# Performance work log

Hardware: AMD Instinct MI355X
Metric: run time of the kernel (lower is better)

The kernel has to match this reference:

```python
import jax, jax.numpy as jnp
import numpy as np

C = 512          # in_channels == key_channels
K_REGIONS = 256  # number of proxy/object regions
N, H, Wd = 8, 128, 128


def _cba(x, w, sc, bi):
    """1x1 Conv + (folded) BN + ReLU. x: [n, Cin, h, w], w: [Cout, Cin]."""
    y = jnp.einsum('nchw,oc->nohw', x, w)
    return jax.nn.relu(sc[None, :, None, None] * y + bi[None, :, None, None])


def setup_inputs() -> dict:
    key = jax.random.key(0)
    kx, kp, kw, ks, kb = jax.random.split(key, 5)
    x = jax.random.normal(kx, (N, C, H, Wd), dtype=jnp.float32)
    proxy = jax.random.normal(kp, (N, C, K_REGIONS, 1), dtype=jnp.float32)
    # 7 ConvBnAct layers: [fp0, fp1, fo0, fo1, fd0, fd1, fup]
    W = jax.random.normal(kw, (7, C, C), dtype=jnp.float32) * (1.0 / np.sqrt(C))
    s = jax.random.uniform(ks, (7, C), dtype=jnp.float32, minval=0.5, maxval=1.5)
    b = jax.random.normal(kb, (7, C), dtype=jnp.float32) * 0.02
    return {'x': x, 'proxy': proxy, 'W': W, 's': s, 'b': b}


def reference(x, proxy, W, s, b):
    n, _, h, w = x.shape
    # f_pixel(x): two 1x1 ConvBnAct -> query [n, HW, C]
    q = _cba(_cba(x, W[0], s[0], b[0]), W[1], s[1], b[1])
    query = q.reshape(n, C, h * w).transpose(0, 2, 1)          # [n, HW, C]
    # f_object(proxy) -> key [n, C, K]
    k = _cba(_cba(proxy, W[2], s[2], b[2]), W[3], s[3], b[3])
    key_t = k.reshape(n, C, -1)                                 # [n, C, K]
    # f_down(proxy) -> value [n, K, C]
    v = _cba(_cba(proxy, W[4], s[4], b[4]), W[5], s[5], b[5])
    value = v.reshape(n, C, -1).transpose(0, 2, 1)              # [n, K, C]
    # scaled dot-product attention (single head, unmasked)
    sim = jnp.einsum('nqc,nck->nqk', query, key_t) * (C ** -0.5)
    sim = jax.nn.softmax(sim, axis=-1)                          # [n, HW, K]
    context = jnp.einsum('nqk,nkc->nqc', sim, value)            # [n, HW, C]
    context = context.transpose(0, 2, 1).reshape(n, C, h, w)
    # f_up
    return _cba(context, W[6], s[6], b[6])
```

## Files before the change

### kernel.cpp

```cpp
#include <hip/hip_runtime.h>
#include <hip/hip_bf16.h>
#include <stdint.h>

typedef __bf16 bf16;
typedef __bf16 bf16x8 __attribute__((ext_vector_type(8)));
typedef __bf16 bf16x4v __attribute__((ext_vector_type(4)));
typedef float f32x4 __attribute__((ext_vector_type(4)));

#define AS1 __attribute__((address_space(1)))
#define AS3 __attribute__((address_space(3)))

__device__ __forceinline__ void g2lds16(const bf16* g, bf16* l) {
  __builtin_amdgcn_global_load_lds((AS1 void*)(uintptr_t)g, (AS3 void*)l, 16, 0, 0);
}

__global__ void prep_weights_k(const float* __restrict__ W, const float* __restrict__ s,
                               const float* __restrict__ b, bf16* __restrict__ Wb,
                               float* __restrict__ bb, bf16* __restrict__ W24,
                               float* __restrict__ b24) {
  int idx = blockIdx.x * 256 + threadIdx.x;
  int c = idx & 511;
  int o = (idx >> 9) & 511;
  int l = idx >> 18;
  const float r = 0.04419417382415922f;
  float f = (l == 3) ? r : 1.0f;
  float wv = W[idx] * s[(l << 9) + o] * f;
  float bv = b[(l << 9) + o] * f;
  Wb[idx] = (bf16)wv;
  if (c == 0) bb[(l << 9) + o] = bv;
  if (l == 2) { W24[(size_t)o * 512 + c] = (bf16)wv;         if (c == 0) b24[o] = bv; }
  if (l == 4) { W24[(size_t)(512 + o) * 512 + c] = (bf16)wv; if (c == 0) b24[512 + o] = bv; }
}

__global__ void transpose_cast_k(const float* __restrict__ in, bf16* __restrict__ out,
                                 int R, int S) {
  __shared__ float tile[64][65];
  int s0 = blockIdx.x * 64, r0 = blockIdx.y * 64;
  size_t zo = (size_t)blockIdx.z * R * S;
  int t = threadIdx.x;
  int rr = t >> 4, cc = t & 15;
#pragma unroll
  for (int i = 0; i < 4; i++) {
    float4 v = *(const float4*)&in[zo + (size_t)(r0 + rr + 16 * i) * S + s0 + cc * 4];
    tile[rr + 16 * i][cc * 4 + 0] = v.x;
    tile[rr + 16 * i][cc * 4 + 1] = v.y;
    tile[rr + 16 * i][cc * 4 + 2] = v.z;
    tile[rr + 16 * i][cc * 4 + 3] = v.w;
  }
  __syncthreads();
#pragma unroll
  for (int i = 0; i < 4; i++) {
    int sR = rr + 16 * i;
    bf16x4v o;
    o.x = (bf16)tile[cc * 4 + 0][sR];
    o.y = (bf16)tile[cc * 4 + 1][sR];
    o.z = (bf16)tile[cc * 4 + 2][sR];
    o.w = (bf16)tile[cc * 4 + 3][sR];
    *(bf16x4v*)&out[zo + (size_t)(s0 + sR) * R + r0 + cc * 4] = o;
  }
}


#define MFMA16(AF, BF, IO, JO)                                                \
  __builtin_amdgcn_s_setprio(1);                                              \
  _Pragma("unroll") for (int kx = 0; kx < 2; kx++)                            \
  _Pragma("unroll") for (int i = 0; i < 4; i++)                               \
  _Pragma("unroll") for (int j = 0; j < 2; j++)                               \
      acc[(IO) + i][(JO) + j] = __builtin_amdgcn_mfma_f32_16x16x32_bf16(      \
          AF[i][kx], BF[j][kx], acc[(IO) + i][(JO) + j], 0, 0, 0);            \
  __builtin_amdgcn_s_setprio(0);

#define RD_A(DST, BUF, ROFF)                                                  \
  _Pragma("unroll") for (int i = 0; i < 4; i++)                               \
  _Pragma("unroll") for (int kx = 0; kx < 2; kx++) {                          \
    const int ar = wm * 128 + (ROFF) + i * 16 + fr;                           \
    DST[i][kx] = *(const bf16x8*)&sm[BUF][0][ar]                              \
        [(((kx << 2) + fq8) ^ (ar & 7)) << 3];                                \
  }

#define RD_B(DST, BUF, COFF)                                                  \
  _Pragma("unroll") for (int j = 0; j < 2; j++)                               \
  _Pragma("unroll") for (int kx = 0; kx < 2; kx++) {                          \
    const int br = wn * 64 + (COFF) + j * 16 + fr;                            \
    DST[j][kx] = *(const bf16x8*)&sm[BUF][1][br]                              \
        [(((kx << 2) + fq8) ^ (br & 7)) << 3];                                \
  }

#define PH_SYNC_PRE  __builtin_amdgcn_s_barrier(); __builtin_amdgcn_sched_barrier(0);
#define PH_SYNC_POST __builtin_amdgcn_sched_barrier(0); __builtin_amdgcn_s_barrier();

template <bool RELU, bool OUTF32, int BIASMODE>
__global__ __launch_bounds__(512, 2) void gemm_nt(
    const bf16* __restrict__ A, long sAb, int lda,
    const bf16* __restrict__ B, long sBb, int ldb,
    void* __restrict__ OUT, long sOb,
    const float* __restrict__ bias,
    int M, int N, int Kd) {
  __shared__ bf16 sm[2][2][256][64];
  const int t = threadIdx.x;
  const int lane = t & 63;
  const int w = t >> 6;
  const int wm = w >> 2;
  const int wn = w & 3;
  const int n0 = blockIdx.x * 256;
  const int m0 = blockIdx.y * 256;
  const bf16* __restrict__ Ab = A + (size_t)blockIdx.z * sAb;
  const bf16* __restrict__ Bb = B + (size_t)blockIdx.z * sBb;
  const int nk = Kd >> 6;

  const int prow = t >> 3;
  const int pchunk = t & 7;
  const int lch = pchunk ^ (prow & 7);

  const int fr = lane & 15;
  const int fq8 = lane >> 4;

  auto stage = [&](int ab, int h, int kt) {
    const int ktc = (kt < nk) ? kt : 0;
    const bf16* __restrict__ src = ab ? Bb : Ab;
    const int ld = ab ? ldb : lda;
    const int r0 = (ab ? n0 : m0) + h * 128;
    const int buf = kt & 1;
#pragma unroll
    for (int j = 0; j < 2; j++) {
      const int pr = j * 64 + prow;
      g2lds16(src + (size_t)(r0 + pr) * ld + (ktc << 6) + (lch << 3),
              &sm[buf][ab][h * 128 + pr][pchunk << 3]);
    }
  };

  f32x4 acc[8][4] = {};
  bf16x8 a0[4][2], a1[4][2], b0[2][2], b1[2][2];

  stage(0, 0, 0); stage(0, 1, 0); stage(1, 0, 0); stage(1, 1, 0);
  stage(1, 0, 1); stage(1, 1, 1);
  asm volatile("s_waitcnt vmcnt(4)" ::: "memory");
  __builtin_amdgcn_s_barrier();
  __builtin_amdgcn_sched_barrier(0);

  for (int T = 0; T < nk; T += 2) {
    RD_A(a0, 0, 0)
    RD_B(b0, 0, 0)
    stage(0, 0, T + 1);
    PH_SYNC_PRE
    MFMA16(a0, b0, 0, 0)
    PH_SYNC_POST
    RD_B(b1, 0, 32)
    stage(0, 1, T + 1);
    PH_SYNC_PRE
    MFMA16(a0, b1, 0, 2)
    PH_SYNC_POST
    RD_A(a1, 0, 64)
    stage(1, 0, T + 2);
    PH_SYNC_PRE
    MFMA16(a1, b0, 4, 0)
    PH_SYNC_POST
    stage(1, 1, T + 2);
    PH_SYNC_PRE
    MFMA16(a1, b1, 4, 2)
    asm volatile("s_waitcnt vmcnt(4)" ::: "memory");
    PH_SYNC_POST
    RD_A(a0, 1, 0)
    RD_B(b0, 1, 0)
    stage(0, 0, T + 2);
    PH_SYNC_PRE
    MFMA16(a0, b0, 0, 0)
    PH_SYNC_POST
    RD_B(b1, 1, 32)
    stage(0, 1, T + 2);
    PH_SYNC_PRE
    MFMA16(a0, b1, 0, 2)
    PH_SYNC_POST
    RD_A(a1, 1, 64)
    stage(1, 0, T + 3);
    PH_SYNC_PRE
    MFMA16(a1, b0, 4, 0)
    PH_SYNC_POST
    stage(1, 1, T + 3);
    PH_SYNC_PRE
    MFMA16(a1, b1, 4, 2)
    asm volatile("s_waitcnt vmcnt(4)" ::: "memory");
    PH_SYNC_POST
  }

  asm volatile("s_waitcnt vmcnt(0)" ::: "memory");

  const int rb = m0 + wm * 128 + (fq8 << 2);
  const int cb = n0 + wn * 64 + fr;
#pragma unroll
  for (int i = 0; i < 8; i++) {
#pragma unroll
    for (int r = 0; r < 4; r++) {
      const int orow = rb + i * 16 + r;
#pragma unroll
      for (int j = 0; j < 4; j++) {
        const int oc = cb + j * 16;
        float vv = acc[i][j][r];
        if (BIASMODE == 1) vv += bias[oc];
        else if (BIASMODE == 2) vv += bias[orow];
        if (RELU) vv = fmaxf(vv, 0.0f);
        if (OUTF32)
          ((float*)OUT)[(size_t)blockIdx.z * sOb + (size_t)orow * N + oc] = vv;
        else
          ((bf16*)OUT)[(size_t)blockIdx.z * sOb + (size_t)orow * N + oc] = (bf16)vv;
      }
    }
  }
}

__global__ __launch_bounds__(256, 2) void sim_softmax_k(
    const bf16* __restrict__ Q, const bf16* __restrict__ Key, bf16* __restrict__ P) {
  __shared__ bf16 sQ[128][64];
  __shared__ bf16 sK[256][64];
  const int t = threadIdx.x;
  const int lane = t & 63;
  const int w = t >> 6;
  const int m0 = blockIdx.x * 128;
  const bf16* Qz = Q + (size_t)blockIdx.y * 16384 * 512;
  const bf16* Kz = Key + (size_t)blockIdx.y * 256 * 512;
  bf16* Pz = P + (size_t)blockIdx.y * 16384 * 256;

  const int fr = lane & 15;
  const int quad = lane >> 4;
  const int fq = quad << 3;
  const int wm = w << 5;
  const int srow = t >> 3;
  const int scol = (t & 7) << 3;

  f32x4 acc[2][16] = {};

  for (int k0 = 0; k0 < 512; k0 += 64) {
#pragma unroll
    for (int i = 0; i < 4; i++)
      g2lds16(Qz + (size_t)(m0 + i * 32 + srow) * 512 + k0 + scol, &sQ[i * 32 + srow][scol]);
#pragma unroll
    for (int i = 0; i < 8; i++)
      g2lds16(Kz + (size_t)(i * 32 + srow) * 512 + k0 + scol, &sK[i * 32 + srow][scol]);
    __syncthreads();
#pragma unroll
    for (int kk = 0; kk < 64; kk += 32) {
      bf16x8 aq0 = *(const bf16x8*)&sQ[wm + fr][kk + fq];
      bf16x8 aq1 = *(const bf16x8*)&sQ[wm + 16 + fr][kk + fq];
#pragma unroll
      for (int j = 0; j < 16; j++) {
        bf16x8 bk = *(const bf16x8*)&sK[j * 16 + fr][kk + fq];
        acc[0][j] = __builtin_amdgcn_mfma_f32_16x16x32_bf16(aq0, bk, acc[0][j], 0, 0, 0);
        acc[1][j] = __builtin_amdgcn_mfma_f32_16x16x32_bf16(aq1, bk, acc[1][j], 0, 0, 0);
      }
    }
    __syncthreads();
  }

#pragma unroll
  for (int i = 0; i < 2; i++) {
#pragma unroll
    for (int r = 0; r < 4; r++) {
      float m = acc[i][0][r];
#pragma unroll
      for (int j = 1; j < 16; j++) m = fmaxf(m, acc[i][j][r]);
#pragma unroll
      for (int o = 1; o < 16; o <<= 1) m = fmaxf(m, __shfl_xor(m, o));
      float sum = 0.0f;
#pragma unroll
      for (int j = 0; j < 16; j++) {
        float e = __expf(acc[i][j][r] - m);
        acc[i][j][r] = e;
        sum += e;
      }
#pragma unroll
      for (int o = 1; o < 16; o <<= 1) sum += __shfl_xor(sum, o);
      float inv = 1.0f / sum;
      const size_t rowoff = (size_t)(m0 + wm + i * 16 + (quad << 2) + r) * 256;
#pragma unroll
      for (int j = 0; j < 16; j++)
        Pz[rowoff + j * 16 + fr] = (bf16)(acc[i][j][r] * inv);
    }
  }
}

extern "C" void kernel_launch(void* const* d_in, const int* in_sizes, int n_in,
                              void* d_out, int out_size, void* d_ws, size_t ws_size,
                              hipStream_t stream) {
  const float* x = (const float*)d_in[0];
  const float* proxy = (const float*)d_in[1];
  const float* W = (const float*)d_in[2];
  const float* s = (const float*)d_in[3];
  const float* b = (const float*)d_in[4];
  float* out = (float*)d_out;

  const int C = 512, K = 256, NB = 8, HW = 16384;
  const size_t MiB = 1024 * 1024;
  char* ws = (char*)d_ws;
  if (ws_size < 272 * MiB) return;

  bf16* Wb   = (bf16*)(ws + 0);
  float* bb  = (float*)(ws + 3670016);
  bf16* W24  = (bf16*)(ws + 4 * MiB);
  float* b24 = (float*)(ws + 5 * MiB);
  bf16* pT   = (bf16*)(ws + 6 * MiB);
  bf16* kt   = (bf16*)(ws + 8 * MiB);
  bf16* key  = (bf16*)(ws + 12 * MiB);
  bf16* v    = (bf16*)(ws + 14 * MiB);
  bf16* bufA = (bf16*)(ws + 16 * MiB);
  bf16* bufB = (bf16*)(ws + 144 * MiB);

  bf16* xb  = bufA;
  bf16* t0  = bufB;
  bf16* q   = bufA;
  bf16* P   = bufB;
  bf16* ctx = bufA;

  const long KC = (long)K * C;
  const long KT = (long)K * 1024;
  const long HWC = (long)HW * C;
  const long HWK = (long)HW * K;

  prep_weights_k<<<7 * 512 * 512 / 256, 256, 0, stream>>>(W, s, b, Wb, bb, W24, b24);
  transpose_cast_k<<<dim3(K / 64, C / 64, NB), 256, 0, stream>>>(proxy, pT, C, K);
  transpose_cast_k<<<dim3(HW / 64, C / 64, NB), 256, 0, stream>>>(x, xb, C, HW);
  gemm_nt<true, false, 1><<<dim3(1024 / 256, K / 256, NB), 512, 0, stream>>>(
      pT, KC, C, W24, 0, C, kt, KT, b24, K, 1024, C);
  gemm_nt<true, false, 1><<<dim3(C / 256, K / 256, NB), 512, 0, stream>>>(
      kt, KT, 1024, Wb + 3 * 262144, 0, C, key, KC, bb + 3 * 512, K, C, C);
  gemm_nt<true, false, 2><<<dim3(K / 256, C / 256, NB), 512, 0, stream>>>(
      Wb + 5 * 262144, 0, C, kt + 512, KT, 1024, v, KC, bb + 5 * 512, C, K, C);
  gemm_nt<true, false, 1><<<dim3(C / 256, HW / 256, NB), 512, 0, stream>>>(
      xb, HWC, C, Wb, 0, C, t0, HWC, bb, HW, C, C);
  gemm_nt<true, false, 1><<<dim3(C / 256, HW / 256, NB), 512, 0, stream>>>(
      t0, HWC, C, Wb + 1 * 262144, 0, C, q, HWC, bb + 512, HW, C, C);
  sim_softmax_k<<<dim3(HW / 128, NB), 256, 0, stream>>>(q, key, P);
  gemm_nt<false, false, 0><<<dim3(C / 256, HW / 256, NB), 512, 0, stream>>>(
      P, HWK, K, v, KC, K, ctx, HWC, nullptr, HW, C, K);
  gemm_nt<true, true, 2><<<dim3(HW / 256, C / 256, NB), 512, 0, stream>>>(
      Wb + 6 * 262144, 0, C, ctx, HWC, C, out, HWC, bb + 6 * 512, C, HW, C);
}
```

Baseline: 894.1 us.

## Pipeline sim-softmax with double-buffered swizzled LDS; use 128-tile GEMMs for proxy

Rewrites the similarity+softmax kernel to use 512 threads over 256 query rows. Q and K tiles are double-buffered in XOR-swizzled LDS and staged asynchronously, interleaved with MFMA phases, using the same phase-sync macros as the main GEMM. Adds a 128x128 tile GEMM for the small proxy-branch GEMMs so they launch more blocks and fill the CUs better. Also widens the transpose-cast stores to 16-byte vectors. This adds LDS pressure and complex waitcnt bookkeeping, and a prefetch past the last K step is clamped to a dummy reload.

```diff
diff --git a/kernel.cpp b/kernel.cpp
--- a/kernel.cpp
+++ b/kernel.cpp
@@ -4,7 +4,6 @@
 
 typedef __bf16 bf16;
 typedef __bf16 bf16x8 __attribute__((ext_vector_type(8)));
-typedef __bf16 bf16x4v __attribute__((ext_vector_type(4)));
 typedef float f32x4 __attribute__((ext_vector_type(4)));
 
 #define AS1 __attribute__((address_space(1)))
@@ -48,16 +47,14 @@
     tile[rr + 16 * i][cc * 4 + 3] = v.w;
   }
   __syncthreads();
-#pragma unroll
-  for (int i = 0; i < 4; i++) {
-    int sR = rr + 16 * i;
-    bf16x4v o;
-    o.x = (bf16)tile[cc * 4 + 0][sR];
-    o.y = (bf16)tile[cc * 4 + 1][sR];
-    o.z = (bf16)tile[cc * 4 + 2][sR];
-    o.w = (bf16)tile[cc * 4 + 3][sR];
-    *(bf16x4v*)&out[zo + (size_t)(s0 + sR) * R + r0 + cc * 4] = o;
-  }
+  const int sr = t >> 2, rg = t & 3;
+  bf16x8 o0, o1;
+#pragma unroll
+  for (int e = 0; e < 8; e++) o0[e] = (bf16)tile[rg * 16 + e][sr];
+#pragma unroll
+  for (int e = 0; e < 8; e++) o1[e] = (bf16)tile[rg * 16 + 8 + e][sr];
+  *(bf16x8*)&out[zo + (size_t)(s0 + sr) * R + r0 + rg * 16] = o0;
+  *(bf16x8*)&out[zo + (size_t)(s0 + sr) * R + r0 + rg * 16 + 8] = o1;
 }
 
 
@@ -208,48 +205,188 @@
   }
 }
 
-__global__ __launch_bounds__(256, 2) void sim_softmax_k(
-    const bf16* __restrict__ Q, const bf16* __restrict__ Key, bf16* __restrict__ P) {
-  __shared__ bf16 sQ[128][64];
-  __shared__ bf16 sK[256][64];
+template <bool RELU, bool OUTF32, int BIASMODE>
+__global__ __launch_bounds__(256, 2) void gemm_nt128(
+    const bf16* __restrict__ A, long sAb, int lda,
+    const bf16* __restrict__ B, long sBb, int ldb,
+    void* __restrict__ OUT, long sOb,
+    const float* __restrict__ bias,
+    int M, int N, int Kd) {
+  __shared__ bf16 sA[128][64];
+  __shared__ bf16 sB[128][64];
+  const int n0 = blockIdx.x * 128;
+  const int m0 = blockIdx.y * 128;
+  const bf16* Ab = A + (size_t)blockIdx.z * sAb;
+  const bf16* Bb = B + (size_t)blockIdx.z * sBb;
   const int t = threadIdx.x;
   const int lane = t & 63;
   const int w = t >> 6;
-  const int m0 = blockIdx.x * 128;
+  const int wm = (w & 1) << 6;
+  const int wn = (w >> 1) << 6;
+  const int srow = t >> 3;
+  const int scol = (t & 7) << 3;
+
+  f32x4 acc[4][4] = {};
+  const int fr = lane & 15;
+  const int fq = (lane >> 4) << 3;
+
+  for (int k0 = 0; k0 < Kd; k0 += 64) {
+#pragma unroll
+    for (int i = 0; i < 4; i++) {
+      g2lds16(Ab + (size_t)(m0 + i * 32 + srow) * lda + (k0 + scol), &sA[i * 32 + srow][scol]);
+      g2lds16(Bb + (size_t)(n0 + i * 32 + srow) * ldb + (k0 + scol), &sB[i * 32 + srow][scol]);
+    }
+    __syncthreads();
+#pragma unroll
+    for (int kk = 0; kk < 64; kk += 32) {
+      bf16x8 af[4], bfv[4];
+#pragma unroll
+      for (int i = 0; i < 4; i++) af[i] = *(const bf16x8*)&sA[wm + i * 16 + fr][kk + fq];
+#pragma unroll
+      for (int j = 0; j < 4; j++) bfv[j] = *(const bf16x8*)&sB[wn + j * 16 + fr][kk + fq];
+#pragma unroll
+      for (int i = 0; i < 4; i++)
+#pragma unroll
+        for (int j = 0; j < 4; j++)
+          acc[i][j] = __builtin_amdgcn_mfma_f32_16x16x32_bf16(af[i], bfv[j], acc[i][j], 0, 0, 0);
+    }
+    __syncthreads();
+  }
+
+  const int rb = m0 + wm + ((lane >> 4) << 2);
+  const int cb = n0 + wn + (lane & 15);
+#pragma unroll
+  for (int i = 0; i < 4; i++) {
+#pragma unroll
+    for (int r = 0; r < 4; r++) {
+      const int orow = rb + i * 16 + r;
+#pragma unroll
+      for (int j = 0; j < 4; j++) {
+        const int oc = cb + j * 16;
+        float vv = acc[i][j][r];
+        if (BIASMODE == 1) vv += bias[oc];
+        else if (BIASMODE == 2) vv += bias[orow];
+        if (RELU) vv = fmaxf(vv, 0.0f);
+        if (OUTF32)
+          ((float*)OUT)[(size_t)blockIdx.z * sOb + (size_t)orow * N + oc] = vv;
+        else
+          ((bf16*)OUT)[(size_t)blockIdx.z * sOb + (size_t)orow * N + oc] = (bf16)vv;
+      }
+    }
+  }
+}
+
+
+#define SIM_AQ(BUF)                                                           \
+  _Pragma("unroll") for (int i2 = 0; i2 < 2; i2++)                            \
+  _Pragma("unroll") for (int kx = 0; kx < 2; kx++) {                          \
+    const int ar = wm + i2 * 16 + fr;                                         \
+    aq[i2][kx] = *(const bf16x8*)&sm[BUF][0][ar]                              \
+        [(((kx << 2) + quad) ^ (ar & 7)) << 3];                               \
+  }
+
+#define SIM_BK(BUF, JQ)                                                       \
+  _Pragma("unroll") for (int jj = 0; jj < 4; jj++)                            \
+  _Pragma("unroll") for (int kx = 0; kx < 2; kx++) {                          \
+    const int br = (JQ) * 64 + jj * 16 + fr;                                  \
+    bk[jj][kx] = *(const bf16x8*)&sm[BUF][1][br]                              \
+        [(((kx << 2) + quad) ^ (br & 7)) << 3];                               \
+  }
+
+#define SIM_MM(JQ)                                                            \
+  __builtin_amdgcn_s_setprio(1);                                              \
+  _Pragma("unroll") for (int kx = 0; kx < 2; kx++)                            \
+  _Pragma("unroll") for (int jj = 0; jj < 4; jj++)                            \
+  _Pragma("unroll") for (int i2 = 0; i2 < 2; i2++)                            \
+    acc[i2][(JQ) * 4 + jj] = __builtin_amdgcn_mfma_f32_16x16x32_bf16(         \
+        aq[i2][kx], bk[jj][kx], acc[i2][(JQ) * 4 + jj], 0, 0, 0);             \
+  __builtin_amdgcn_s_setprio(0);
+
+__global__ __launch_bounds__(512, 2) void sim_softmax_k(
+    const bf16* __restrict__ Q, const bf16* __restrict__ Key, bf16* __restrict__ P) {
+  __shared__ bf16 sm[2][2][256][64];
+  const int t = threadIdx.x;
+  const int lane = t & 63;
+  const int w = t >> 6;
+  const int m0 = blockIdx.x * 256;
   const bf16* Qz = Q + (size_t)blockIdx.y * 16384 * 512;
   const bf16* Kz = Key + (size_t)blockIdx.y * 256 * 512;
   bf16* Pz = P + (size_t)blockIdx.y * 16384 * 256;
 
   const int fr = lane & 15;
   const int quad = lane >> 4;
-  const int fq = quad << 3;
   const int wm = w << 5;
-  const int srow = t >> 3;
-  const int scol = (t & 7) << 3;
+  const int prow = t >> 3;
+  const int pchunk = t & 7;
+  const int lch = pchunk ^ (prow & 7);
+  const int nk = 8;
+
+  auto stage = [&](int ab, int u, int kt) {
+    const int ktc = (kt < nk) ? kt : 0;
+    const bf16* __restrict__ src = ab ? Kz : Qz;
+    const int r0 = (ab ? 0 : m0) + u * 64;
+    g2lds16(src + (size_t)(r0 + prow) * 512 + (ktc << 6) + (lch << 3),
+            &sm[kt & 1][ab][u * 64 + prow][pchunk << 3]);
+  };
 
   f32x4 acc[2][16] = {};
-
-  for (int k0 = 0; k0 < 512; k0 += 64) {
-#pragma unroll
-    for (int i = 0; i < 4; i++)
-      g2lds16(Qz + (size_t)(m0 + i * 32 + srow) * 512 + k0 + scol, &sQ[i * 32 + srow][scol]);
-#pragma unroll
-    for (int i = 0; i < 8; i++)
-      g2lds16(Kz + (size_t)(i * 32 + srow) * 512 + k0 + scol, &sK[i * 32 + srow][scol]);
-    __syncthreads();
-#pragma unroll
-    for (int kk = 0; kk < 64; kk += 32) {
-      bf16x8 aq0 = *(const bf16x8*)&sQ[wm + fr][kk + fq];
-      bf16x8 aq1 = *(const bf16x8*)&sQ[wm + 16 + fr][kk + fq];
-#pragma unroll
-      for (int j = 0; j < 16; j++) {
-        bf16x8 bk = *(const bf16x8*)&sK[j * 16 + fr][kk + fq];
-        acc[0][j] = __builtin_amdgcn_mfma_f32_16x16x32_bf16(aq0, bk, acc[0][j], 0, 0, 0);
-        acc[1][j] = __builtin_amdgcn_mfma_f32_16x16x32_bf16(aq1, bk, acc[1][j], 0, 0, 0);
-      }
-    }
-    __syncthreads();
-  }
+  bf16x8 aq[2][2], bk[4][2];
+
+  stage(0, 0, 0); stage(0, 1, 0); stage(0, 2, 0); stage(0, 3, 0);
+  stage(1, 0, 0); stage(1, 1, 0); stage(1, 2, 0); stage(1, 3, 0);
+  stage(1, 0, 1); stage(1, 1, 1); stage(1, 2, 1);
+  asm volatile("s_waitcnt vmcnt(3)" ::: "memory");
+  __builtin_amdgcn_s_barrier();
+  __builtin_amdgcn_sched_barrier(0);
+
+  for (int T = 0; T < nk; T += 2) {
+    SIM_AQ(0)
+    SIM_BK(0, 0)
+    stage(1, 3, T + 1); stage(0, 0, T + 1);
+    PH_SYNC_PRE
+    SIM_MM(0)
+    PH_SYNC_POST
+    SIM_BK(0, 1)
+    stage(0, 1, T + 1); stage(0, 2, T + 1);
+    PH_SYNC_PRE
+    SIM_MM(1)
+    PH_SYNC_POST
+    SIM_BK(0, 2)
+    stage(0, 3, T + 1); stage(1, 0, T + 2);
+    PH_SYNC_PRE
+    SIM_MM(2)
+    PH_SYNC_POST
+    SIM_BK(0, 3)
+    stage(1, 1, T + 2); stage(1, 2, T + 2);
+    PH_SYNC_PRE
+    SIM_MM(3)
+    asm volatile("s_waitcnt vmcnt(3)" ::: "memory");
+    PH_SYNC_POST
+    SIM_AQ(1)
+    SIM_BK(1, 0)
+    stage(1, 3, T + 2); stage(0, 0, T + 2);
+    PH_SYNC_PRE
+    SIM_MM(0)
+    PH_SYNC_POST
+    SIM_BK(1, 1)
+    stage(0, 1, T + 2); stage(0, 2, T + 2);
+    PH_SYNC_PRE
+    SIM_MM(1)
+    PH_SYNC_POST
+    SIM_BK(1, 2)
+    stage(0, 3, T + 2); stage(1, 0, T + 3);
+    PH_SYNC_PRE
+    SIM_MM(2)
+    PH_SYNC_POST
+    SIM_BK(1, 3)
+    stage(1, 1, T + 3); stage(1, 2, T + 3);
+    PH_SYNC_PRE
+    SIM_MM(3)
+    asm volatile("s_waitcnt vmcnt(3)" ::: "memory");
+    PH_SYNC_POST
+  }
+
+  asm volatile("s_waitcnt vmcnt(0)" ::: "memory");
 
 #pragma unroll
   for (int i = 0; i < 2; i++) {
@@ -318,17 +455,17 @@
   prep_weights_k<<<7 * 512 * 512 / 256, 256, 0, stream>>>(W, s, b, Wb, bb, W24, b24);
   transpose_cast_k<<<dim3(K / 64, C / 64, NB), 256, 0, stream>>>(proxy, pT, C, K);
   transpose_cast_k<<<dim3(HW / 64, C / 64, NB), 256, 0, stream>>>(x, xb, C, HW);
-  gemm_nt<true, false, 1><<<dim3(1024 / 256, K / 256, NB), 512, 0, stream>>>(
+  gemm_nt128<true, false, 1><<<dim3(1024 / 128, K / 128, NB), 256, 0, stream>>>(
       pT, KC, C, W24, 0, C, kt, KT, b24, K, 1024, C);
-  gemm_nt<true, false, 1><<<dim3(C / 256, K / 256, NB), 512, 0, stream>>>(
+  gemm_nt128<true, false, 1><<<dim3(C / 128, K / 128, NB), 256, 0, stream>>>(
       kt, KT, 1024, Wb + 3 * 262144, 0, C, key, KC, bb + 3 * 512, K, C, C);
-  gemm_nt<true, false, 2><<<dim3(K / 256, C / 256, NB), 512, 0, stream>>>(
+  gemm_nt128<true, false, 2><<<dim3(K / 128, C / 128, NB), 256, 0, stream>>>(
       Wb + 5 * 262144, 0, C, kt + 512, KT, 1024, v, KC, bb + 5 * 512, C, K, C);
   gemm_nt<true, false, 1><<<dim3(C / 256, HW / 256, NB), 512, 0, stream>>>(
       xb, HWC, C, Wb, 0, C, t0, HWC, bb, HW, C, C);
   gemm_nt<true, false, 1><<<dim3(C / 256, HW / 256, NB), 512, 0, stream>>>(
       t0, HWC, C, Wb + 1 * 262144, 0, C, q, HWC, bb + 512, HW, C, C);
-  sim_softmax_k<<<dim3(HW / 128, NB), 256, 0, stream>>>(q, key, P);
+  sim_softmax_k<<<dim3(HW / 256, NB), 512, 0, stream>>>(q, key, P);
   gemm_nt<false, false, 0><<<dim3(C / 256, HW / 256, NB), 512, 0, stream>>>(
       P, HWK, K, v, KC, K, ctx, HWC, nullptr, HW, C, K);
   gemm_nt<true, true, 2><<<dim3(HW / 256, C / 256, NB), 512, 0, stream>>>(
```

Measured after the change: 873.3 us. 1.02x faster.
